# Performance work log

Hardware: AMD Instinct MI355X
Metric: run time of the kernel (lower is better)

## Reference

```python
import jax, jax.numpy as jnp
import numpy as np
import math

N = 100000      # nodes
E = 1600000     # edges
F_IN = 256      # num_features
H = 64          # num_hidden
C = 64          # num_classes
L = 8           # num_layers
ALPHA = 0.5
THETA = 1.0


def setup_inputs() -> dict:
    key = jax.random.key(0)
    ks = jax.random.split(key, 7)
    x = jax.random.normal(ks[0], (N, F_IN), dtype=jnp.float32)
    edge_index = jax.random.randint(ks[1], (2, E), 0, N, dtype=jnp.int64)
    w_in = jax.random.normal(ks[2], (F_IN, H), dtype=jnp.float32) / np.float32(math.sqrt(F_IN))
    b_in = jnp.zeros((H,), dtype=jnp.float32)
    w_layers = jax.random.normal(ks[3], (L, H, H), dtype=jnp.float32) / np.float32(math.sqrt(H))
    w_out = jax.random.normal(ks[4], (H, C), dtype=jnp.float32) / np.float32(math.sqrt(H))
    b_out = jnp.zeros((C,), dtype=jnp.float32)
    return {"x": x, "edge_index": edge_index, "w_in": w_in, "b_in": b_in,
            "w_layers": w_layers, "w_out": w_out, "b_out": b_out}


def reference(x, edge_index, w_in, b_in, w_layers, w_out, b_out):
    # --- gcn_norm: add self loops, symmetric D^-1/2 (A+I) D^-1/2 ---
    loop = jnp.arange(N, dtype=edge_index.dtype)
    src = jnp.concatenate([edge_index[0], loop])   # [E+N]
    dst = jnp.concatenate([edge_index[1], loop])   # [E+N]
    deg = jax.ops.segment_sum(jnp.ones_like(src, dtype=x.dtype), dst, num_segments=N)
    dinv = jnp.where(deg > 0, jax.lax.rsqrt(jnp.maximum(deg, 1e-12)), 0.0)
    norm = dinv[src] * dinv[dst]                   # [E+N]

    # initial linear + ELU (dropout is identity in eval mode)
    h = jax.nn.elu(x @ w_in + b_in)                # [N, H]
    x0 = h

    for l in range(L):
        beta = math.log(THETA / (l + 1) + 1.0)     # GCN2Conv beta, layer index 1-based
        # sparse neighbor aggregation: P_hat @ h
        agg = jax.ops.segment_sum(norm[:, None] * h[src], dst, num_segments=N)  # [N, H]
        s = (1.0 - ALPHA) * agg + ALPHA * x0       # initial residual
        out = (1.0 - beta) * s + beta * (s @ w_layers[l])  # identity mapping (shared weights)
        h = jax.nn.elu(out) + out                  # elu + residual (dropout off)

    return h @ w_out + b_out                       # [N, C]
```

## Files before the change

### kernel.cpp

```cpp
#include <hip/hip_runtime.h>
#include <hip/hip_fp16.h>
#include <math.h>

#define NN 100000
#define EE 1600000
#define HH 64
#define LL 8
#define NBLK ((NN + 1023) / 1024)
#define AGG_BLOCKS 2496

#define NPB 512
#define BSH 9
#define NBUCK ((NN + NPB - 1) / NPB)
#define BIN_CHUNK 4096

typedef _Float16 f16x8 __attribute__((ext_vector_type(8)));
typedef float f32x4 __attribute__((ext_vector_type(4)));

__device__ __forceinline__ float eluf(float x) { return x > 0.0f ? x : expm1f(x); }


__global__ void count_edges_v2(const int* __restrict__ dst, int* __restrict__ counts) {
    int i = blockIdx.x * blockDim.x + threadIdx.x;
    if (i < EE) atomicAdd(&counts[dst[i]], 1);
}

__global__ void scan_block_v2(const int* __restrict__ counts, int* __restrict__ rp,
                              int* __restrict__ partial, float* __restrict__ dinv) {
    __shared__ int sm[256];
    const int t = threadIdx.x;
    const int base = blockIdx.x * 1024 + t * 4;
    int v0 = 0, v1 = 0, v2 = 0, v3 = 0;
    if (base + 0 < NN) v0 = counts[base + 0];
    if (base + 1 < NN) v1 = counts[base + 1];
    if (base + 2 < NN) v2 = counts[base + 2];
    if (base + 3 < NN) v3 = counts[base + 3];
    if (base + 0 < NN) dinv[base + 0] = rsqrtf((float)(v0 + 1));
    if (base + 1 < NN) dinv[base + 1] = rsqrtf((float)(v1 + 1));
    if (base + 2 < NN) dinv[base + 2] = rsqrtf((float)(v2 + 1));
    if (base + 3 < NN) dinv[base + 3] = rsqrtf((float)(v3 + 1));
    const int s = v0 + v1 + v2 + v3;
    sm[t] = s;
    __syncthreads();
    for (int off = 1; off < 256; off <<= 1) {
        int x = 0;
        if (t >= off) x = sm[t - off];
        __syncthreads();
        if (t >= off) sm[t] += x;
        __syncthreads();
    }
    int excl = sm[t] - s;
    if (t == 255) partial[blockIdx.x] = sm[255];
    if (base + 0 < NN) rp[base + 0] = excl;
    excl += v0;
    if (base + 1 < NN) rp[base + 1] = excl;
    excl += v1;
    if (base + 2 < NN) rp[base + 2] = excl;
    excl += v2;
    if (base + 3 < NN) rp[base + 3] = excl;
}

__global__ void scan_top_v2(int* partial) {
    __shared__ int sm[128];
    const int t = threadIdx.x;
    const int v = (t < NBLK) ? partial[t] : 0;
    sm[t] = v;
    __syncthreads();
    for (int off = 1; off < 128; off <<= 1) {
        int x = 0;
        if (t >= off) x = sm[t - off];
        __syncthreads();
        if (t >= off) sm[t] += x;
        __syncthreads();
    }
    if (t < NBLK) partial[t] = sm[t] - v;
}

__global__ void scan_add_v2(int* rp, const int* __restrict__ partial) {
    const int i = blockIdx.x * blockDim.x + threadIdx.x;
    if (i < NN) rp[i] += partial[i >> 10];
    else if (i == NN) rp[NN] = EE;
}


__global__ __launch_bounds__(256) void bin_edges_v1(const int* __restrict__ src,
                                                    const int* __restrict__ dst,
                                                    const int* __restrict__ rp,
                                                    int* __restrict__ bfill,
                                                    unsigned* __restrict__ tmp) {
    __shared__ int hist[NBUCK];
    __shared__ int basei[NBUCK];
    __shared__ int rpb[NBUCK];
    __shared__ int cur[NBUCK];
    const int t = threadIdx.x;
    const int e0 = blockIdx.x * BIN_CHUNK;
    for (int b = t; b < NBUCK; b += 256) {
        hist[b] = 0;
        cur[b] = 0;
    }
    __syncthreads();
    int myd[16];
#pragma unroll
    for (int i = 0; i < 16; ++i) {
        const int e = e0 + i * 256 + t;
        int d = -1;
        if (e < EE) {
            d = dst[e];
            atomicAdd(&hist[d >> BSH], 1);
        }
        myd[i] = d;
    }
    __syncthreads();
    for (int b = t; b < NBUCK; b += 256) {
        const int h = hist[b];
        basei[b] = h ? atomicAdd(&bfill[b], h) : 0;
        rpb[b] = rp[b << BSH];
    }
    __syncthreads();
#pragma unroll
    for (int i = 0; i < 16; ++i) {
        const int e = e0 + i * 256 + t;
        if (e < EE) {
            const int d = myd[i];
            const int b = d >> BSH;
            const int slot = atomicAdd(&cur[b], 1);
            tmp[rpb[b] + basei[b] + slot] =
                ((unsigned)(d & (NPB - 1)) << 17) | (unsigned)src[e];
        }
    }
}

__global__ __launch_bounds__(512) void unbin_v1(const unsigned* __restrict__ tmp,
                                                const int* __restrict__ rp,
                                                int* __restrict__ col) {
    __shared__ int lrp[NPB];
    __shared__ int lfill[NPB];
    const int t = threadIdx.x;
    const int node0 = blockIdx.x << BSH;
    const int nodes = (NN - node0 < NPB) ? (NN - node0) : NPB;
    for (int i = t; i < nodes; i += 512) {
        lrp[i] = rp[node0 + i];
        lfill[i] = 0;
    }
    __syncthreads();
    const int lo = rp[node0];
    const int hi = rp[node0 + nodes];
    for (int e = lo + t; e < hi; e += 512) {
        const unsigned v = tmp[e];
        const int s = (int)(v & 0x1FFFFu);
        const int doff = (int)(v >> 17);
        const int pos = lrp[doff] + atomicAdd(&lfill[doff], 1);
        col[pos] = s;
    }
}

__global__ void init_sent_v2(__half* a, __half* b) {
    const int t = threadIdx.x;
    if (t < 64) a[(size_t)NN * HH + t] = __float2half(0.f);
    else b[(size_t)NN * HH + (t - 64)] = __float2half(0.f);
}

__global__ void conv_w_v1(const float* __restrict__ w, __half* __restrict__ wt) {
    const int t = threadIdx.x;
    const int c = t & 63;
    const int k0 = (t >> 6) * 64;
    for (int k = 0; k < 64; ++k)
        wt[(size_t)c * 256 + k0 + k] = __float2half(w[(size_t)(k0 + k) * 64 + c]);
}

__global__ void conv_wbl_v1(const float* __restrict__ w_layers, __half* __restrict__ btab) {
    const int l = blockIdx.x;
    const float beta = logf(1.0f / (float)(l + 1) + 1.0f);
    const float* W = w_layers + (size_t)l * 64 * 64;
    __half* wt = btab + (size_t)l * 64 * 64;
    const int t = threadIdx.x;
    const int c = t & 63;
    const int k0 = (t >> 6) * 16;
    for (int k = k0; k < k0 + 16; ++k)
        wt[(size_t)c * 64 + k] = __float2half(beta * W[(size_t)k * 64 + c]);
}


__global__ __launch_bounds__(256) void agg_v2(
    const int* __restrict__ rp, const int* __restrict__ col, const float* __restrict__ dinv,
    const __half* __restrict__ hin, const float* __restrict__ x0, float* __restrict__ sout) {
    const int lane = threadIdx.x & 63;
    const int g = lane >> 3;
    const int fc = (lane & 7) << 3;
    const int wave = blockIdx.x * 4 + (threadIdx.x >> 6);
    const int nwaves = gridDim.x * 4;

    for (int node = wave; node < NN; node += nwaves) {
        const int start = rp[node], end = rp[node + 1];
        float acc[8] = {};
        for (int e = start; e < end; e += 64) {
            const int me = e + lane;
            const int c = (me < end) ? col[me] : NN;
            int nb = end - e;
            if (nb > 64) nb = 64;
            const int it = (nb + 31) >> 5;
            for (int j = 0; j < it; ++j) {
                const int b = j * 32 + g;
                const int c0 = __shfl(c, b, 64);
                const int c1 = __shfl(c, b + 8, 64);
                const int c2 = __shfl(c, b + 16, 64);
                const int c3 = __shfl(c, b + 24, 64);
                float4 r0 = *(const float4*)(hin + ((size_t)c0 << 6) + fc);
                float4 r1 = *(const float4*)(hin + ((size_t)c1 << 6) + fc);
                float4 r2 = *(const float4*)(hin + ((size_t)c2 << 6) + fc);
                float4 r3 = *(const float4*)(hin + ((size_t)c3 << 6) + fc);
                const __half2* h0 = (const __half2*)&r0;
                const __half2* h1 = (const __half2*)&r1;
                const __half2* h2 = (const __half2*)&r2;
                const __half2* h3 = (const __half2*)&r3;
#pragma unroll
                for (int q = 0; q < 4; ++q) {
                    const float2 f0 = __half22float2(h0[q]);
                    const float2 f1 = __half22float2(h1[q]);
                    const float2 f2 = __half22float2(h2[q]);
                    const float2 f3 = __half22float2(h3[q]);
                    acc[2 * q] += (f0.x + f1.x) + (f2.x + f3.x);
                    acc[2 * q + 1] += (f0.y + f1.y) + (f2.y + f3.y);
                }
            }
        }
#pragma unroll
        for (int m = 8; m <= 32; m <<= 1)
#pragma unroll
            for (int q = 0; q < 8; ++q) acc[q] += __shfl_xor(acc[q], m, 64);
        if (g == 0) {
            float4 r = *(const float4*)(hin + ((size_t)node << 6) + fc);
            const __half2* hh = (const __half2*)&r;
#pragma unroll
            for (int q = 0; q < 4; ++q) {
                const float2 f = __half22float2(hh[q]);
                acc[2 * q] += f.x;
                acc[2 * q + 1] += f.y;
            }
            const float di = dinv[node];
            const float4* xp = (const float4*)(x0 + ((size_t)node << 6) + fc);
            const float4 xa = xp[0], xb = xp[1];
            float4 oa, ob;
            oa.x = 0.5f * fmaf(di, acc[0], xa.x);
            oa.y = 0.5f * fmaf(di, acc[1], xa.y);
            oa.z = 0.5f * fmaf(di, acc[2], xa.z);
            oa.w = 0.5f * fmaf(di, acc[3], xa.w);
            ob.x = 0.5f * fmaf(di, acc[4], xb.x);
            ob.y = 0.5f * fmaf(di, acc[5], xb.y);
            ob.z = 0.5f * fmaf(di, acc[6], xb.z);
            ob.w = 0.5f * fmaf(di, acc[7], xb.w);
            float4* sp = (float4*)(sout + ((size_t)node << 6) + fc);
            sp[0] = oa;
            sp[1] = ob;
        }
    }
}


__global__ __launch_bounds__(256, 4) void mgemm_in_v1(
    const float* __restrict__ A, const __half* __restrict__ wt,
    const float* __restrict__ bias, const float* __restrict__ dinvp,
    float* __restrict__ out32, __half* __restrict__ out16) {
    __shared__ __half sh[64][264];
    const int t = threadIdx.x;
    const int row0 = blockIdx.x * 64;

#pragma unroll
    for (int i = 0; i < 16; ++i) {
        const int linear = t + i * 256;
        const int r = linear >> 6;
        const int q = linear & 63;
        const int grow = row0 + r;
        float4 v = make_float4(0.f, 0.f, 0.f, 0.f);
        if (grow < NN) v = *(const float4*)&A[(size_t)grow * 256 + q * 4];
        __half2* dst = (__half2*)&sh[r][q * 4];
        dst[0] = __floats2half2_rn(v.x, v.y);
        dst[1] = __floats2half2_rn(v.z, v.w);
    }
    __syncthreads();

    const int lane = t & 63;
    const int w = t >> 6;
    const int la = lane & 15, lg = lane >> 4;
    f32x4 acc[4] = {};
    const __half* arow = &sh[w * 16 + la][0];
#pragma unroll
    for (int kc = 0; kc < 8; ++kc) {
        const int k0 = kc * 32 + lg * 8;
        const f16x8 a = *(const f16x8*)&arow[k0];
#pragma unroll
        for (int tt = 0; tt < 4; ++tt) {
            const f16x8 b = *(const f16x8*)&wt[(size_t)(la + 16 * tt) * 256 + k0];
            acc[tt] = __builtin_amdgcn_mfma_f32_16x16x32_f16(a, b, acc[tt], 0, 0, 0);
        }
    }

#pragma unroll
    for (int i = 0; i < 4; ++i) {
        const int r = row0 + w * 16 + lg * 4 + i;
        if (r >= NN) continue;
        const float dv = dinvp[r];
#pragma unroll
        for (int tt = 0; tt < 4; ++tt) {
            const int c = la + 16 * tt;
            float o = acc[tt][i] + bias[c];
            o = eluf(o);
            out32[(size_t)r * 64 + c] = o;
            out16[(size_t)r * 64 + c] = __float2half(o * dv);
        }
    }
}


__global__ __launch_bounds__(256, 8) void lgemm_v5(
    const float* __restrict__ S, const __half* __restrict__ wt, float obeta,
    const float* __restrict__ dinvp, __half* __restrict__ out16,
    float* __restrict__ out32, int w32) {
    __shared__ float sa[64][68];
    const int t = threadIdx.x;
    const int row0 = blockIdx.x * 64;

#pragma unroll
    for (int i = 0; i < 4; ++i) {
        const int linear = t + i * 256;
        const int r = linear >> 4, q = linear & 15;
        const int grow = row0 + r;
        float4 v = make_float4(0.f, 0.f, 0.f, 0.f);
        if (grow < NN) v = *(const float4*)&S[(size_t)grow * 64 + q * 4];
        *(float4*)&sa[r][q * 4] = v;
    }
    __syncthreads();

    const int lane = t & 63;
    const int w = t >> 6;
    const int la = lane & 15, lg = lane >> 4;
    f32x4 acc[4] = {};
    const float* arow = &sa[w * 16 + la][0];
#pragma unroll
    for (int kc = 0; kc < 2; ++kc) {
        const int k0 = kc * 32 + lg * 8;
        const float4 s0 = *(const float4*)&arow[k0];
        const float4 s1 = *(const float4*)&arow[k0 + 4];
        f16x8 a;
        a[0] = (_Float16)s0.x; a[1] = (_Float16)s0.y;
        a[2] = (_Float16)s0.z; a[3] = (_Float16)s0.w;
        a[4] = (_Float16)s1.x; a[5] = (_Float16)s1.y;
        a[6] = (_Float16)s1.z; a[7] = (_Float16)s1.w;
#pragma unroll
        for (int tt = 0; tt < 4; ++tt) {
            const f16x8 b = *(const f16x8*)&wt[(size_t)(la + 16 * tt) * 64 + k0];
            acc[tt] = __builtin_amdgcn_mfma_f32_16x16x32_f16(a, b, acc[tt], 0, 0, 0);
        }
    }

#pragma unroll
    for (int i = 0; i < 4; ++i) {
        const int lr = w * 16 + lg * 4 + i;
        const int r = row0 + lr;
        if (r >= NN) continue;
        const float dv = dinvp[r];
#pragma unroll
        for (int tt = 0; tt < 4; ++tt) {
            const int c = la + 16 * tt;
            const float o = acc[tt][i] + obeta * sa[lr][c];
            const float h = eluf(o) + o;
            out16[(size_t)r * 64 + c] = __float2half(h * dv);
            if (w32) out32[(size_t)r * 64 + c] = h;
        }
    }
}


template <int KTOT, int MODE>
__global__ __launch_bounds__(256, 4) void gemm_v2(const float* __restrict__ A,
                                                  const float* __restrict__ B,
                                                  const float* __restrict__ bias,
                                                  const float* __restrict__ dinvp,
                                                  float* __restrict__ out32,
                                                  __half* __restrict__ out16) {
    __shared__ float ss[64][68];
    __shared__ float ws[64][64];
    const int t = threadIdx.x;
    const int row0 = blockIdx.x * 64;
    const int tx = t & 15, ty = t >> 4;
    float acc[4][4] = {};

    for (int kc = 0; kc < KTOT; kc += 64) {
#pragma unroll
        for (int i = 0; i < 4; ++i) {
            const int linear = t + i * 256;
            const int r = linear >> 4, q = linear & 15;
            const int grow = row0 + r;
            float4 v = make_float4(0.f, 0.f, 0.f, 0.f);
            if (grow < NN) v = *(const float4*)&A[(size_t)grow * KTOT + kc + q * 4];
            *(float4*)&ss[r][q * 4] = v;
        }
#pragma unroll
        for (int i = 0; i < 4; ++i) {
            const int linear = t + i * 256;
            const int r = linear >> 4, q = linear & 15;
            *(float4*)&ws[r][q * 4] = *(const float4*)&B[(size_t)(kc + r) * 64 + q * 4];
        }
        __syncthreads();
#pragma unroll 4
        for (int k = 0; k < 64; k += 4) {
            float4 af[4], bf[4];
            af[0] = *(const float4*)&ss[ty * 4 + 0][k];
            af[1] = *(const float4*)&ss[ty * 4 + 1][k];
            af[2] = *(const float4*)&ss[ty * 4 + 2][k];
            af[3] = *(const float4*)&ss[ty * 4 + 3][k];
            bf[0] = *(const float4*)&ws[k + 0][tx * 4];
            bf[1] = *(const float4*)&ws[k + 1][tx * 4];
            bf[2] = *(const float4*)&ws[k + 2][tx * 4];
            bf[3] = *(const float4*)&ws[k + 3][tx * 4];
            const float* A4 = (const float*)af;
            const float* B4 = (const float*)bf;
#pragma unroll
            for (int i = 0; i < 4; ++i)
#pragma unroll
                for (int kk = 0; kk < 4; ++kk)
#pragma unroll
                    for (int j = 0; j < 4; ++j)
                        acc[i][j] = fmaf(A4[i * 4 + kk], B4[kk * 4 + j], acc[i][j]);
        }
        __syncthreads();
    }

#pragma unroll
    for (int i = 0; i < 4; ++i) {
        const int r = row0 + ty * 4 + i;
        if (r >= NN) continue;
        float4 o;
        float* op = (float*)&o;
#pragma unroll
        for (int j = 0; j < 4; ++j) {
            float xv = acc[i][j] + bias[tx * 4 + j];
            if (MODE == 0) xv = eluf(xv);
            op[j] = xv;
        }
        *(float4*)&out32[(size_t)r * 64 + tx * 4] = o;
        if (MODE == 0) {
            const float dv = dinvp[r];
            __half2* hp = (__half2*)&out16[(size_t)r * 64 + tx * 4];
            hp[0] = __floats2half2_rn(o.x * dv, o.y * dv);
            hp[1] = __floats2half2_rn(o.z * dv, o.w * dv);
        }
    }
}


extern "C" void kernel_launch(void* const* d_in, const int* in_sizes, int n_in, void* d_out,
                              int out_size, void* d_ws, size_t ws_size, hipStream_t stream) {
    const float* x = (const float*)d_in[0];
    const int* ei = (const int*)d_in[1];
    const float* w_in = (const float*)d_in[2];
    const float* b_in = (const float*)d_in[3];
    const float* w_layers = (const float*)d_in[4];
    const float* w_out = (const float*)d_in[5];
    const float* b_out = (const float*)d_in[6];
    float* out = (float*)d_out;

    char* p = (char*)d_ws;
    auto alloc = [&](size_t bytes) -> char* {
        char* r = p;
        p += (bytes + 255) & ~(size_t)255;
        return r;
    };
    int* counts = (int*)alloc((size_t)NN * 4);
    int* bfill = (int*)alloc((size_t)NBUCK * 4);
    int* rp = (int*)alloc((size_t)(NN + 1) * 4);
    int* partial = (int*)alloc(128 * 4);
    float* dinv = (float*)alloc((size_t)NN * 4);
    int* colA = (int*)alloc((size_t)EE * 4);
    unsigned* tmp = (unsigned*)alloc((size_t)EE * 4);
    float* x0 = (float*)alloc((size_t)NN * HH * 4);
    __half* x0h = (__half*)alloc((size_t)(NN + 1) * HH * 2);
    __half* hA = (__half*)alloc((size_t)(NN + 1) * HH * 2);
    float* sbuf = (float*)alloc((size_t)NN * HH * 4);
    __half* wt = (__half*)alloc((size_t)64 * 256 * 2);
    __half* btab = (__half*)alloc((size_t)LL * 64 * 64 * 2);

    const int* srcA = ei;
    const int* dstA = ei + EE;

    hipMemsetAsync(counts, 0, (size_t)NN * 4, stream);
    hipMemsetAsync(bfill, 0, (size_t)NBUCK * 4, stream);
    init_sent_v2<<<1, 128, 0, stream>>>(x0h, hA);
    conv_w_v1<<<1, 256, 0, stream>>>(w_in, wt);
    conv_wbl_v1<<<LL, 256, 0, stream>>>(w_layers, btab);
    count_edges_v2<<<(EE + 255) / 256, 256, 0, stream>>>(dstA, counts);
    scan_block_v2<<<NBLK, 256, 0, stream>>>(counts, rp, partial, dinv);
    scan_top_v2<<<1, 128, 0, stream>>>(partial);
    scan_add_v2<<<(NN + 1 + 255) / 256, 256, 0, stream>>>(rp, partial);
    bin_edges_v1<<<(EE + BIN_CHUNK - 1) / BIN_CHUNK, 256, 0, stream>>>(srcA, dstA, rp, bfill,
                                                                       tmp);
    unbin_v1<<<NBUCK, 512, 0, stream>>>(tmp, rp, colA);

    mgemm_in_v1<<<(NN + 63) / 64, 256, 0, stream>>>(x, wt, b_in, dinv, x0, x0h);

    for (int l = 0; l < LL; ++l) {
        const float beta = (float)log(1.0 / (double)(l + 1) + 1.0);
        const float obeta = 1.0f - beta;
        const __half* hin = (l & 1) ? hA : x0h;
        __half* hout = (l & 1) ? x0h : hA;
        agg_v2<<<AGG_BLOCKS, 256, 0, stream>>>(rp, colA, dinv, hin, x0, sbuf);
        lgemm_v5<<<(NN + 63) / 64, 256, 0, stream>>>(sbuf, btab + (size_t)l * 64 * 64, obeta,
                                                     dinv, hout, sbuf, l == LL - 1);
    }
    gemm_v2<64, 2><<<(NN + 63) / 64, 256, 0, stream>>>(sbuf, w_out, b_out, nullptr, out, nullptr);
}
```

Baseline: 850.1 us.

## Map each node to an 8-lane group in aggregation; split input GEMM K-staging

The aggregation kernel now gives each 8-lane group its own node, so one wave handles 8 nodes. Each group loads its column indices directly, four neighbors per step, instead of a whole wave looping over one node with shuffles and a cross-lane reduction. This targets poor lane utilization on low-degree nodes (average degree about 16) and the cost of the reduction. The input GEMM stages A through shared memory in two K-halves with a smaller buffer and a launch-bounds hint of 6, aiming for higher occupancy at the cost of an extra barrier round.

```diff
diff --git a/kernel.cpp b/kernel.cpp
--- a/kernel.cpp
+++ b/kernel.cpp
@@ -7,7 +7,7 @@
 #define HH 64
 #define LL 8
 #define NBLK ((NN + 1023) / 1024)
-#define AGG_BLOCKS 2496
+#define AGG3_BLOCKS ((NN + 31) / 32)
 
 #define NPB 512
 #define BSH 9
@@ -181,118 +181,108 @@
 }
 
 
-__global__ __launch_bounds__(256) void agg_v2(
+__global__ __launch_bounds__(256) void agg_v3(
     const int* __restrict__ rp, const int* __restrict__ col, const float* __restrict__ dinv,
     const __half* __restrict__ hin, const float* __restrict__ x0, float* __restrict__ sout) {
     const int lane = threadIdx.x & 63;
     const int g = lane >> 3;
     const int fc = (lane & 7) << 3;
-    const int wave = blockIdx.x * 4 + (threadIdx.x >> 6);
-    const int nwaves = gridDim.x * 4;
-
-    for (int node = wave; node < NN; node += nwaves) {
-        const int start = rp[node], end = rp[node + 1];
-        float acc[8] = {};
-        for (int e = start; e < end; e += 64) {
-            const int me = e + lane;
-            const int c = (me < end) ? col[me] : NN;
-            int nb = end - e;
-            if (nb > 64) nb = 64;
-            const int it = (nb + 31) >> 5;
-            for (int j = 0; j < it; ++j) {
-                const int b = j * 32 + g;
-                const int c0 = __shfl(c, b, 64);
-                const int c1 = __shfl(c, b + 8, 64);
-                const int c2 = __shfl(c, b + 16, 64);
-                const int c3 = __shfl(c, b + 24, 64);
-                float4 r0 = *(const float4*)(hin + ((size_t)c0 << 6) + fc);
-                float4 r1 = *(const float4*)(hin + ((size_t)c1 << 6) + fc);
-                float4 r2 = *(const float4*)(hin + ((size_t)c2 << 6) + fc);
-                float4 r3 = *(const float4*)(hin + ((size_t)c3 << 6) + fc);
-                const __half2* h0 = (const __half2*)&r0;
-                const __half2* h1 = (const __half2*)&r1;
-                const __half2* h2 = (const __half2*)&r2;
-                const __half2* h3 = (const __half2*)&r3;
-#pragma unroll
-                for (int q = 0; q < 4; ++q) {
-                    const float2 f0 = __half22float2(h0[q]);
-                    const float2 f1 = __half22float2(h1[q]);
-                    const float2 f2 = __half22float2(h2[q]);
-                    const float2 f3 = __half22float2(h3[q]);
-                    acc[2 * q] += (f0.x + f1.x) + (f2.x + f3.x);
-                    acc[2 * q + 1] += (f0.y + f1.y) + (f2.y + f3.y);
-                }
-            }
-        }
-#pragma unroll
-        for (int m = 8; m <= 32; m <<= 1)
-#pragma unroll
-            for (int q = 0; q < 8; ++q) acc[q] += __shfl_xor(acc[q], m, 64);
-        if (g == 0) {
-            float4 r = *(const float4*)(hin + ((size_t)node << 6) + fc);
-            const __half2* hh = (const __half2*)&r;
-#pragma unroll
-            for (int q = 0; q < 4; ++q) {
-                const float2 f = __half22float2(hh[q]);
-                acc[2 * q] += f.x;
-                acc[2 * q + 1] += f.y;
-            }
-            const float di = dinv[node];
-            const float4* xp = (const float4*)(x0 + ((size_t)node << 6) + fc);
-            const float4 xa = xp[0], xb = xp[1];
-            float4 oa, ob;
-            oa.x = 0.5f * fmaf(di, acc[0], xa.x);
-            oa.y = 0.5f * fmaf(di, acc[1], xa.y);
-            oa.z = 0.5f * fmaf(di, acc[2], xa.z);
-            oa.w = 0.5f * fmaf(di, acc[3], xa.w);
-            ob.x = 0.5f * fmaf(di, acc[4], xb.x);
-            ob.y = 0.5f * fmaf(di, acc[5], xb.y);
-            ob.z = 0.5f * fmaf(di, acc[6], xb.z);
-            ob.w = 0.5f * fmaf(di, acc[7], xb.w);
-            float4* sp = (float4*)(sout + ((size_t)node << 6) + fc);
-            sp[0] = oa;
-            sp[1] = ob;
-        }
-    }
-}
-
-
-__global__ __launch_bounds__(256, 4) void mgemm_in_v1(
+    const int wid = blockIdx.x * 4 + (threadIdx.x >> 6);
+    const int node = wid * 8 + g;
+    if (node >= NN) return;
+
+    const int start = rp[node], end = rp[node + 1];
+    float acc[8] = {};
+    for (int e = start; e < end; e += 4) {
+        const int c0 = col[e];
+        const int c1 = (e + 1 < end) ? col[e + 1] : NN;
+        const int c2 = (e + 2 < end) ? col[e + 2] : NN;
+        const int c3 = (e + 3 < end) ? col[e + 3] : NN;
+        float4 r0 = *(const float4*)(hin + ((size_t)c0 << 6) + fc);
+        float4 r1 = *(const float4*)(hin + ((size_t)c1 << 6) + fc);
+        float4 r2 = *(const float4*)(hin + ((size_t)c2 << 6) + fc);
+        float4 r3 = *(const float4*)(hin + ((size_t)c3 << 6) + fc);
+        const __half2* h0 = (const __half2*)&r0;
+        const __half2* h1 = (const __half2*)&r1;
+        const __half2* h2 = (const __half2*)&r2;
+        const __half2* h3 = (const __half2*)&r3;
+#pragma unroll
+        for (int q = 0; q < 4; ++q) {
+            const float2 f0 = __half22float2(h0[q]);
+            const float2 f1 = __half22float2(h1[q]);
+            const float2 f2 = __half22float2(h2[q]);
+            const float2 f3 = __half22float2(h3[q]);
+            acc[2 * q] += (f0.x + f1.x) + (f2.x + f3.x);
+            acc[2 * q + 1] += (f0.y + f1.y) + (f2.y + f3.y);
+        }
+    }
+    {
+        float4 r = *(const float4*)(hin + ((size_t)node << 6) + fc);
+        const __half2* hh = (const __half2*)&r;
+#pragma unroll
+        for (int q = 0; q < 4; ++q) {
+            const float2 f = __half22float2(hh[q]);
+            acc[2 * q] += f.x;
+            acc[2 * q + 1] += f.y;
+        }
+        const float di = dinv[node];
+        const float4* xp = (const float4*)(x0 + ((size_t)node << 6) + fc);
+        const float4 xa = xp[0], xb = xp[1];
+        float4 oa, ob;
+        oa.x = 0.5f * fmaf(di, acc[0], xa.x);
+        oa.y = 0.5f * fmaf(di, acc[1], xa.y);
+        oa.z = 0.5f * fmaf(di, acc[2], xa.z);
+        oa.w = 0.5f * fmaf(di, acc[3], xa.w);
+        ob.x = 0.5f * fmaf(di, acc[4], xb.x);
+        ob.y = 0.5f * fmaf(di, acc[5], xb.y);
+        ob.z = 0.5f * fmaf(di, acc[6], xb.z);
+        ob.w = 0.5f * fmaf(di, acc[7], xb.w);
+        float4* sp = (float4*)(sout + ((size_t)node << 6) + fc);
+        sp[0] = oa;
+        sp[1] = ob;
+    }
+}
+
+
+__global__ __launch_bounds__(256, 6) void mgemm_in_v2(
     const float* __restrict__ A, const __half* __restrict__ wt,
     const float* __restrict__ bias, const float* __restrict__ dinvp,
     float* __restrict__ out32, __half* __restrict__ out16) {
-    __shared__ __half sh[64][264];
+    __shared__ __half sh[64][136];
     const int t = threadIdx.x;
     const int row0 = blockIdx.x * 64;
-
-#pragma unroll
-    for (int i = 0; i < 16; ++i) {
-        const int linear = t + i * 256;
-        const int r = linear >> 6;
-        const int q = linear & 63;
-        const int grow = row0 + r;
-        float4 v = make_float4(0.f, 0.f, 0.f, 0.f);
-        if (grow < NN) v = *(const float4*)&A[(size_t)grow * 256 + q * 4];
-        __half2* dst = (__half2*)&sh[r][q * 4];
-        dst[0] = __floats2half2_rn(v.x, v.y);
-        dst[1] = __floats2half2_rn(v.z, v.w);
-    }
-    __syncthreads();
-
     const int lane = t & 63;
     const int w = t >> 6;
     const int la = lane & 15, lg = lane >> 4;
     f32x4 acc[4] = {};
-    const __half* arow = &sh[w * 16 + la][0];
-#pragma unroll
-    for (int kc = 0; kc < 8; ++kc) {
-        const int k0 = kc * 32 + lg * 8;
-        const f16x8 a = *(const f16x8*)&arow[k0];
-#pragma unroll
-        for (int tt = 0; tt < 4; ++tt) {
-            const f16x8 b = *(const f16x8*)&wt[(size_t)(la + 16 * tt) * 256 + k0];
-            acc[tt] = __builtin_amdgcn_mfma_f32_16x16x32_f16(a, b, acc[tt], 0, 0, 0);
-        }
+
+#pragma unroll
+    for (int kh = 0; kh < 2; ++kh) {
+#pragma unroll
+        for (int i = 0; i < 8; ++i) {
+            const int linear = t + i * 256;
+            const int r = linear >> 5;
+            const int q = linear & 31;
+            const int grow = row0 + r;
+            float4 v = make_float4(0.f, 0.f, 0.f, 0.f);
+            if (grow < NN) v = *(const float4*)&A[(size_t)grow * 256 + kh * 128 + q * 4];
+            __half2* dst = (__half2*)&sh[r][q * 4];
+            dst[0] = __floats2half2_rn(v.x, v.y);
+            dst[1] = __floats2half2_rn(v.z, v.w);
+        }
+        __syncthreads();
+        const __half* arow = &sh[w * 16 + la][0];
+#pragma unroll
+        for (int kc = 0; kc < 4; ++kc) {
+            const int k0 = kc * 32 + lg * 8;
+            const f16x8 a = *(const f16x8*)&arow[k0];
+#pragma unroll
+            for (int tt = 0; tt < 4; ++tt) {
+                const f16x8 b = *(const f16x8*)&wt[(size_t)(la + 16 * tt) * 256 + kh * 128 + k0];
+                acc[tt] = __builtin_amdgcn_mfma_f32_16x16x32_f16(a, b, acc[tt], 0, 0, 0);
+            }
+        }
+        __syncthreads();
     }
 
 #pragma unroll
@@ -496,14 +486,13 @@
                                                                        tmp);
     unbin_v1<<<NBUCK, 512, 0, stream>>>(tmp, rp, colA);
 
-    mgemm_in_v1<<<(NN + 63) / 64, 256, 0, stream>>>(x, wt, b_in, dinv, x0, x0h);
+    mgemm_in_v2<<<(NN + 63) / 64, 256, 0, stream>>>(x, wt, b_in, dinv, x0, x0h);
 
     for (int l = 0; l < LL; ++l) {
-        const float beta = (float)log(1.0 / (double)(l + 1) + 1.0);
-        const float obeta = 1.0f - beta;
+        const float obeta = 1.0f - (float)log(1.0 / (double)(l + 1) + 1.0);
         const __half* hin = (l & 1) ? hA : x0h;
         __half* hout = (l & 1) ? x0h : hA;
-        agg_v2<<<AGG_BLOCKS, 256, 0, stream>>>(rp, colA, dinv, hin, x0, sbuf);
+        agg_v3<<<AGG3_BLOCKS, 256, 0, stream>>>(rp, colA, dinv, hin, x0, sbuf);
         lgemm_v5<<<(NN + 63) / 64, 256, 0, stream>>>(sbuf, btab + (size_t)l * 64 * 64, obeta,
                                                      dinv, hout, sbuf, l == LL - 1);
     }
```

After: 765.2 us. -10.0%, faster.
